# Performance work log

Hardware: AMD Instinct MI355X
Metric: run time of the kernel (lower is better)

Reference implementation:

```python
import jax, jax.numpy as jnp
import numpy as np

DIM = 256
N_EMBED = 2048
EPS_LOG = 1e-07


def setup_inputs() -> dict:
    key = jax.random.key(0)
    k_in, k_emb = jax.random.split(key)
    inp = jax.random.normal(k_in, (16, 64, 64, DIM), dtype=jnp.float32)
    # embeddings_initial_variance = 1 -> plain randn
    embed = jax.random.normal(k_emb, (DIM, N_EMBED), dtype=jnp.float32)
    return {"input": inp, "embed": embed}


def reference(input, embed):
    # Eval-mode forward of Quantize (no EMA buffer updates).
    flatten = input.reshape(-1, DIM)                      # [N, dim]
    # squared euclidean distance via expansion:
    dist = (
        jnp.sum(flatten * flatten, axis=1, keepdims=True)
        - 2.0 * (flatten @ embed)
        + jnp.sum(embed * embed, axis=0, keepdims=True)
    )
    embed_ind_flat = jnp.argmax(-dist, axis=1)            # [N] int
    embed_ind = embed_ind_flat.reshape(input.shape[:-1])  # [B,H,W]

    # gather codes: F.embedding(embed_ind, embed.T)
    quantize = jnp.take(embed.T, embed_ind, axis=0)       # [B,H,W,dim]

    # commitment loss with detached quantize
    diff = jnp.mean((jax.lax.stop_gradient(quantize) - input) ** 2)

    # straight-through estimator
    quantize_st = input + jax.lax.stop_gradient(quantize - input)

    # perplexity from average code assignment probabilities
    n = flatten.shape[0]
    counts = jnp.zeros((N_EMBED,), dtype=flatten.dtype).at[embed_ind_flat].add(1.0)
    avg_probas = counts / n
    perplexity = jnp.exp(
        -jnp.sum(avg_probas * jnp.log(jnp.clip(avg_probas, EPS_LOG, None)))
    )
    return quantize_st, diff, embed_ind, perplexity
```

## Files before the change

### kernel.cpp

```cpp
#include <hip/hip_runtime.h>
#include <cstdint>
#include <cstddef>

#define DIM    256
#define NE     2048
#define NROWS  65536

#define OFF_DIFF ((size_t)16777216)
#define OFF_IND  ((size_t)16777217)
#define OFF_PERP ((size_t)16842753)

#define WS_DIFF   0
#define WS_CNT    64
#define WS_EN     8256
#define WS_ET     16448
#define WS_BPH    2113600
#define WS_BPL    3162176
#define WS_NEED_V2 ((size_t)4210752)
#define WS_ET_NEED ((size_t)2113600)

typedef __attribute__((ext_vector_type(8))) _Float16 half8;
typedef __attribute__((ext_vector_type(4))) float    float4v;

__device__ __forceinline__ float4v mfma16(half8 a, half8 b, float4v c) {
    return __builtin_amdgcn_mfma_f32_16x16x32_f16(a, b, c, 0, 0, 0);
}

__device__ __forceinline__ void gld16(const void* g, void* l) {
    __builtin_amdgcn_global_load_lds((const __attribute__((address_space(1))) void*)g,
                                     (__attribute__((address_space(3))) void*)l,
                                     16, 0, 0);
}


__global__ __launch_bounds__(256) void k_prep(const float* __restrict__ embed,
                                              float* __restrict__ enorm) {
    int j = blockIdx.x * 256 + threadIdx.x;
    double s = 0.0;
    for (int d = 0; d < DIM; ++d) {
        float e = embed[(size_t)d * NE + j];
        s += (double)e * (double)e;
    }
    enorm[j] = (float)s;
}

__global__ __launch_bounds__(256) void k_transpose(const float* __restrict__ embed,
                                                   float* __restrict__ embedT) {
    int j0 = blockIdx.x * 8;
    for (int jj = 0; jj < 8; ++jj) {
        int j = j0 + jj;
        embedT[(size_t)j * DIM + threadIdx.x] = embed[(size_t)threadIdx.x * NE + j];
    }
}

__global__ __launch_bounds__(256) void k_pack(const float* __restrict__ embed,
                                              _Float16* __restrict__ bph,
                                              _Float16* __restrict__ bpl) {
    int t   = blockIdx.x * 256 + threadIdx.x;
    int col = t & (NE - 1);
    int kg  = t >> 11;
    half8 h, l;
#pragma unroll
    for (int j = 0; j < 8; ++j) {
        float e = embed[(size_t)(kg * 8 + j) * NE + col];
        _Float16 eh = (_Float16)e;
        h[j] = eh;
        l[j] = (_Float16)(e - (float)eh);
    }
    size_t idx = (size_t)(col >> 5) * 1024 + (size_t)kg * 32 + (size_t)(col & 31);
    *(half8*)(bph + idx * 8) = h;
    *(half8*)(bpl + idx * 8) = l;
}


__device__ __forceinline__ void stage_chunk(const char* srch, const char* srcl,
                                            char* dst, int w, int lane) {
#pragma unroll
    for (int s = 0; s < 4; ++s) {
        int seg = w * 4 + s;
        gld16(srch + seg * 1024 + lane * 16, dst + seg * 1024);
        gld16(srcl + seg * 1024 + lane * 16, dst + 16384 + seg * 1024);
    }
}

__global__ __launch_bounds__(256, 2) void k_gemm(
    const float* __restrict__ inp,
    const _Float16* __restrict__ bph,
    const _Float16* __restrict__ bpl,
    const float* __restrict__ enorm,
    const float* __restrict__ embedT,
    float* __restrict__ out,
    int* __restrict__ counts,
    double* __restrict__ diffacc)
{
    __shared__ __align__(16) char ldsB[2][32768];
    const int tid  = threadIdx.x;
    const int w    = tid >> 6;
    const int lane = tid & 63;
    const int q    = lane >> 4;
    const int nl   = lane & 15;
    const int m0   = blockIdx.x * 128;
    const int mw   = m0 + w * 32;

    half8 ah[2][8], al[2][8];
#pragma unroll
    for (int mf = 0; mf < 2; ++mf) {
        const float* xr = inp + (size_t)(mw + mf * 16 + nl) * DIM + q * 8;
#pragma unroll
        for (int c = 0; c < 8; ++c) {
            float4 f0 = *(const float4*)(xr + c * 32);
            float4 f1 = *(const float4*)(xr + c * 32 + 4);
            float fs[8] = {f0.x, f0.y, f0.z, f0.w, f1.x, f1.y, f1.z, f1.w};
            half8 hh, ll;
#pragma unroll
            for (int j = 0; j < 8; ++j) {
                _Float16 xh = (_Float16)fs[j];
                hh[j] = xh;
                ll[j] = (_Float16)(fs[j] - (float)xh);
            }
            ah[mf][c] = hh;
            al[mf][c] = ll;
        }
    }

    float sv1[2][4], sv2[2][4];
    int   si1[2][4], si2[2][4];
#pragma unroll
    for (int mf = 0; mf < 2; ++mf)
#pragma unroll
        for (int r = 0; r < 4; ++r) {
            sv1[mf][r] = -3.4e38f; sv2[mf][r] = -3.4e38f;
            si1[mf][r] = 0;        si2[mf][r] = 0;
        }

    stage_chunk((const char*)bph, (const char*)bpl, &ldsB[0][0], w, lane);
    __syncthreads();

    for (int nc = 0; nc < 64; ++nc) {
        int pn = nc & 1;
        if (nc < 63)
            stage_chunk((const char*)bph + (size_t)(nc + 1) * 16384,
                        (const char*)bpl + (size_t)(nc + 1) * 16384,
                        &ldsB[pn ^ 1][0], w, lane);

        const char* bb = &ldsB[pn][0] + q * 512 + nl * 16;
        float4v acc[2][2];
#pragma unroll
        for (int mf = 0; mf < 2; ++mf)
#pragma unroll
            for (int nf = 0; nf < 2; ++nf)
                acc[mf][nf] = (float4v){0.f, 0.f, 0.f, 0.f};

#pragma unroll
        for (int c = 0; c < 8; ++c) {
            half8 bh0 = *(const half8*)(bb + c * 2048);
            half8 bh1 = *(const half8*)(bb + c * 2048 + 256);
            half8 bl0 = *(const half8*)(bb + 16384 + c * 2048);
            half8 bl1 = *(const half8*)(bb + 16384 + c * 2048 + 256);
            acc[0][0] = mfma16(ah[0][c], bh0, acc[0][0]);
            acc[1][0] = mfma16(ah[1][c], bh0, acc[1][0]);
            acc[0][1] = mfma16(ah[0][c], bh1, acc[0][1]);
            acc[1][1] = mfma16(ah[1][c], bh1, acc[1][1]);
            acc[0][0] = mfma16(al[0][c], bh0, acc[0][0]);
            acc[1][0] = mfma16(al[1][c], bh0, acc[1][0]);
            acc[0][1] = mfma16(al[0][c], bh1, acc[0][1]);
            acc[1][1] = mfma16(al[1][c], bh1, acc[1][1]);
            acc[0][0] = mfma16(ah[0][c], bl0, acc[0][0]);
            acc[1][0] = mfma16(ah[1][c], bl0, acc[1][0]);
            acc[0][1] = mfma16(ah[0][c], bl1, acc[0][1]);
            acc[1][1] = mfma16(ah[1][c], bl1, acc[1][1]);
        }

        int colb = nc * 32;
#pragma unroll
        for (int nf = 0; nf < 2; ++nf) {
            int col = colb + nf * 16 + nl;
            float en05 = -0.5f * enorm[col];
#pragma unroll
            for (int mf = 0; mf < 2; ++mf) {
#pragma unroll
                for (int r = 0; r < 4; ++r) {
                    float s  = acc[mf][nf][r] + en05;
                    bool g1  = (s > sv1[mf][r]);
                    bool g2  = (s > sv2[mf][r]);
                    float nb2 = g1 ? sv1[mf][r] : (g2 ? s   : sv2[mf][r]);
                    int   ni2 = g1 ? si1[mf][r] : (g2 ? col : si2[mf][r]);
                    sv1[mf][r] = g1 ? s   : sv1[mf][r];
                    si1[mf][r] = g1 ? col : si1[mf][r];
                    sv2[mf][r] = nb2;
                    si2[mf][r] = ni2;
                }
            }
        }
        __syncthreads();
    }

#pragma unroll
    for (int mf = 0; mf < 2; ++mf)
#pragma unroll
        for (int r = 0; r < 4; ++r) {
            float v1 = sv1[mf][r], v2 = sv2[mf][r];
            int   i1 = si1[mf][r], i2 = si2[mf][r];
#pragma unroll
            for (int msk = 1; msk < 16; msk <<= 1) {
                float ov1 = __shfl_xor(v1, msk); int oi1 = __shfl_xor(i1, msk);
                float ov2 = __shfl_xor(v2, msk); int oi2 = __shfl_xor(i2, msk);
                bool afirst = (v1 > ov1) || (v1 == ov1 && i1 < oi1);
                float cv = afirst ? ov1 : v1;  int ci = afirst ? oi1 : i1;
                float sv = afirst ? v2  : ov2; int si = afirst ? i2  : oi2;
                v1 = afirst ? v1 : ov1;        i1 = afirst ? i1 : oi1;
                bool sfirst = (sv > cv) || (sv == cv && si < ci);
                v2 = sfirst ? sv : cv;         i2 = sfirst ? si : ci;
            }
            si1[mf][r] = i1;
            si2[mf][r] = i2;
        }

    double dsum = 0.0;
#pragma unroll
    for (int mf = 0; mf < 2; ++mf)
#pragma unroll
        for (int qq = 0; qq < 4; ++qq)
#pragma unroll
            for (int r = 0; r < 4; ++r) {
                int i1 = __shfl(si1[mf][r], qq * 16);
                int i2 = __shfl(si2[mf][r], qq * 16);
                int row = mw + mf * 16 + qq * 4 + r;
                float4 xv = *(const float4*)(inp    + (size_t)row * DIM + lane * 4);
                float4 e1 = *(const float4*)(embedT + (size_t)i1  * DIM + lane * 4);
                float4 e2 = *(const float4*)(embedT + (size_t)i2  * DIM + lane * 4);
                float d1 = xv.x * e1.x + xv.y * e1.y + xv.z * e1.z + xv.w * e1.w;
                float d2 = xv.x * e2.x + xv.y * e2.y + xv.z * e2.z + xv.w * e2.w;
#pragma unroll
                for (int msk = 1; msk < 64; msk <<= 1) {
                    d1 += __shfl_xor(d1, msk);
                    d2 += __shfl_xor(d2, msk);
                }
                float s1 = 2.f * d1 - enorm[i1];
                float s2 = 2.f * d2 - enorm[i2];
                bool take2 = (s2 > s1) || (s2 == s1 && i2 < i1);
                int win = take2 ? i2 : i1;
                float4 qv = take2 ? e2 : e1;
                *(float4*)(out + (size_t)row * DIM + lane * 4) = qv;
                float dx = qv.x - xv.x, dy = qv.y - xv.y;
                float dz = qv.z - xv.z, dw = qv.w - xv.w;
                dsum += (double)(dx * dx + dy * dy + dz * dz + dw * dw);
                if (lane == 0) {
                    out[OFF_IND + row] = (float)win;
                    atomicAdd(&counts[win], 1);
                }
            }
#pragma unroll
    for (int msk = 1; msk < 64; msk <<= 1) dsum += __shfl_xor(dsum, msk);
    if (lane == 0) atomicAdd(diffacc, dsum);
}

__global__ __launch_bounds__(256) void k_main(const float* __restrict__ inp,
                                              const float* __restrict__ embed,
                                              const float* __restrict__ enorm,
                                              const float* __restrict__ embedT,
                                              int useT,
                                              float* __restrict__ out,
                                              int* __restrict__ counts,
                                              double* __restrict__ diffacc) {
    __shared__ float XsT[DIM][64];
    const int tid = threadIdx.x;
    const int m0  = blockIdx.x * 64;
#pragma unroll
    for (int i = 0; i < 16; ++i) {
        int f = tid + 256 * i;
        int row = f >> 6, c4 = f & 63;
        float4 v = *(const float4*)&inp[(size_t)(m0 + row) * DIM + c4 * 4];
        XsT[c4 * 4 + 0][row] = v.x; XsT[c4 * 4 + 1][row] = v.y;
        XsT[c4 * 4 + 2][row] = v.z; XsT[c4 * 4 + 3][row] = v.w;
    }
    __syncthreads();
    const int tx = tid & 15, ty = tid >> 4;
    float bv[4]; int bi[4];
#pragma unroll
    for (int mi = 0; mi < 4; ++mi) { bv[mi] = -1e30f; bi[mi] = 0x7fffffff; }
    for (int n0 = 0; n0 < NE; n0 += 64) {
        float acc[4][4] = {};
        const float* bp = embed + n0 + tx * 4;
        const float* ap = &XsT[0][ty * 4];
#pragma unroll 8
        for (int k = 0; k < DIM; ++k) {
            float4 b4 = *(const float4*)(bp + (size_t)k * NE);
            float4 a4 = *(const float4*)(ap + k * 64);
            acc[0][0] = fmaf(a4.x, b4.x, acc[0][0]); acc[0][1] = fmaf(a4.x, b4.y, acc[0][1]);
            acc[0][2] = fmaf(a4.x, b4.z, acc[0][2]); acc[0][3] = fmaf(a4.x, b4.w, acc[0][3]);
            acc[1][0] = fmaf(a4.y, b4.x, acc[1][0]); acc[1][1] = fmaf(a4.y, b4.y, acc[1][1]);
            acc[1][2] = fmaf(a4.y, b4.z, acc[1][2]); acc[1][3] = fmaf(a4.y, b4.w, acc[1][3]);
            acc[2][0] = fmaf(a4.z, b4.x, acc[2][0]); acc[2][1] = fmaf(a4.z, b4.y, acc[2][1]);
            acc[2][2] = fmaf(a4.z, b4.z, acc[2][2]); acc[2][3] = fmaf(a4.z, b4.w, acc[2][3]);
            acc[3][0] = fmaf(a4.w, b4.x, acc[3][0]); acc[3][1] = fmaf(a4.w, b4.y, acc[3][1]);
            acc[3][2] = fmaf(a4.w, b4.z, acc[3][2]); acc[3][3] = fmaf(a4.w, b4.w, acc[3][3]);
        }
        float4 en4 = *(const float4*)&enorm[n0 + tx * 4];
        int c0 = n0 + tx * 4;
#pragma unroll
        for (int mi = 0; mi < 4; ++mi) {
            float s0 = 2.f * acc[mi][0] - en4.x, s1 = 2.f * acc[mi][1] - en4.y;
            float s2 = 2.f * acc[mi][2] - en4.z, s3 = 2.f * acc[mi][3] - en4.w;
            float v = s0; int idx = c0;
            if (s1 > v) { v = s1; idx = c0 + 1; }
            if (s2 > v) { v = s2; idx = c0 + 2; }
            if (s3 > v) { v = s3; idx = c0 + 3; }
#pragma unroll
            for (int o = 1; o < 16; o <<= 1) {
                float ov = __shfl_xor(v, o, 64); int oi = __shfl_xor(idx, o, 64);
                if (ov > v || (ov == v && oi < idx)) { v = ov; idx = oi; }
            }
            if (v > bv[mi] || (v == bv[mi] && idx < bi[mi])) { bv[mi] = v; bi[mi] = idx; }
        }
    }
    __syncthreads();
    int* sidx = (int*)&XsT[0][0];
    if (tx == 0) {
#pragma unroll
        for (int mi = 0; mi < 4; ++mi) {
            int rl = ty * 4 + mi; int idx = bi[mi];
            sidx[rl] = idx;
            out[OFF_IND + m0 + rl] = (float)idx;
            atomicAdd(&counts[idx], 1);
        }
    }
    __syncthreads();
    float dsum = 0.f;
    for (int rl = 0; rl < 64; ++rl) {
        int idx = sidx[rl];
        float qv = useT ? embedT[(size_t)idx * DIM + tid] : embed[(size_t)tid * NE + idx];
        float x = inp[(size_t)(m0 + rl) * DIM + tid];
        out[(size_t)(m0 + rl) * DIM + tid] = qv;
        float d = qv - x;
        dsum = fmaf(d, d, dsum);
    }
    double ds = (double)dsum;
#pragma unroll
    for (int o = 32; o > 0; o >>= 1) ds += __shfl_down(ds, o, 64);
    double* red = (double*)&XsT[4][0];
    if ((tid & 63) == 0) red[tid >> 6] = ds;
    __syncthreads();
    if (tid == 0) atomicAdd(diffacc, red[0] + red[1] + red[2] + red[3]);
}

__global__ __launch_bounds__(256) void k_fin(const int* __restrict__ counts,
                                             const double* __restrict__ diffacc,
                                             float* __restrict__ out) {
    __shared__ double red[4];
    int tid = threadIdx.x;
    double s = 0.0;
    for (int i = tid; i < NE; i += 256) {
        int c = counts[i];
        if (c > 0) {
            float p = (float)c * (1.0f / 65536.0f);
            s += (double)(p * logf(p));
        }
    }
#pragma unroll
    for (int o = 32; o > 0; o >>= 1) s += __shfl_down(s, o, 64);
    if ((tid & 63) == 0) red[tid >> 6] = s;
    __syncthreads();
    if (tid == 0) {
        double t = red[0] + red[1] + red[2] + red[3];
        out[OFF_PERP] = expf((float)(-t));
        out[OFF_DIFF] = (float)(diffacc[0] * (1.0 / 16777216.0));
    }
}

extern "C" void kernel_launch(void* const* d_in, const int* in_sizes, int n_in,
                              void* d_out, int out_size, void* d_ws, size_t ws_size,
                              hipStream_t stream) {
    (void)in_sizes; (void)n_in; (void)out_size;
    const float* inp   = (const float*)d_in[0];
    const float* embed = (const float*)d_in[1];
    float* out = (float*)d_out;
    char*  ws  = (char*)d_ws;

    double*   diffacc = (double*)(ws + WS_DIFF);
    int*      counts  = (int*)(ws + WS_CNT);
    float*    enorm   = (float*)(ws + WS_EN);
    float*    embedT  = (float*)(ws + WS_ET);
    _Float16* bph     = (_Float16*)(ws + WS_BPH);
    _Float16* bpl     = (_Float16*)(ws + WS_BPL);

    hipMemsetAsync(d_ws, 0, 8256, stream);
    k_prep<<<NE / 256, 256, 0, stream>>>(embed, enorm);

    if (ws_size >= WS_NEED_V2) {
        k_transpose<<<DIM, 256, 0, stream>>>(embed, embedT);
        k_pack<<<NE * 32 / 256, 256, 0, stream>>>(embed, bph, bpl);
        k_gemm<<<NROWS / 128, 256, 0, stream>>>(inp, bph, bpl, enorm, embedT,
                                                out, counts, diffacc);
    } else {
        int useT = (ws_size >= WS_ET_NEED) ? 1 : 0;
        if (useT) k_transpose<<<DIM, 256, 0, stream>>>(embed, embedT);
        k_main<<<NROWS / 64, 256, 0, stream>>>(inp, embed, enorm,
                                               useT ? embedT : embed, useT,
                                               out, counts, diffacc);
    }
    k_fin<<<1, 256, 0, stream>>>(counts, diffacc, out);
}
```

Measured before the change: 319.9 us.

## Switch GEMM to 32x32x16 MFMA with packed int top-2 argmax and fused pack/transpose

Replaces the 16x16x32 MFMA tiling with 32x32x16 MFMA, so each wave computes a 32x32 tile per chunk with a single accumulator. Fragments are read from a single packed hi/lo buffer. The running top-2 search now packs a quantized score and the column index into one int, which turns compare-and-select into integer max/min operations. The per-code norm offset is precomputed into LDS. The transpose kernel is merged into the pack kernel. The risks are coarse score quantization, which leans on the exact top-2 rescoring, and higher register pressure from 16-element accumulators and 32 A fragments.

```diff
diff --git a/kernel.cpp b/kernel.cpp
--- a/kernel.cpp
+++ b/kernel.cpp
@@ -13,17 +13,16 @@
 #define WS_DIFF   0
 #define WS_CNT    64
 #define WS_EN     8256
-#define WS_ET     16448
-#define WS_BPH    2113600
-#define WS_BPL    3162176
-#define WS_NEED_V2 ((size_t)4210752)
-#define WS_ET_NEED ((size_t)2113600)
-
-typedef __attribute__((ext_vector_type(8))) _Float16 half8;
-typedef __attribute__((ext_vector_type(4))) float    float4v;
-
-__device__ __forceinline__ float4v mfma16(half8 a, half8 b, float4v c) {
-    return __builtin_amdgcn_mfma_f32_16x16x32_f16(a, b, c, 0, 0, 0);
+#define WS_ENC    16448
+#define WS_ET     24640
+#define WS_BPK    2121792
+#define WS_NEED_V2 ((size_t)(2121792 + 2097152))
+
+typedef __attribute__((ext_vector_type(8)))  _Float16 half8;
+typedef __attribute__((ext_vector_type(16))) float    float16v;
+
+__device__ __forceinline__ float16v mfma32(half8 a, half8 b, float16v c) {
+    return __builtin_amdgcn_mfma_f32_32x32x16_f16(a, b, c, 0, 0, 0);
 }
 
 __device__ __forceinline__ void gld16(const void* g, void* l) {
@@ -34,82 +33,72 @@
 
 
 __global__ __launch_bounds__(256) void k_prep(const float* __restrict__ embed,
-                                              float* __restrict__ enorm) {
+                                              float* __restrict__ enorm,
+                                              float* __restrict__ enc) {
     int j = blockIdx.x * 256 + threadIdx.x;
     double s = 0.0;
     for (int d = 0; d < DIM; ++d) {
         float e = embed[(size_t)d * NE + j];
         s += (double)e * (double)e;
     }
-    enorm[j] = (float)s;
-}
-
-__global__ __launch_bounds__(256) void k_transpose(const float* __restrict__ embed,
-                                                   float* __restrict__ embedT) {
-    int j0 = blockIdx.x * 8;
-    for (int jj = 0; jj < 8; ++jj) {
-        int j = j0 + jj;
-        embedT[(size_t)j * DIM + threadIdx.x] = embed[(size_t)threadIdx.x * NE + j];
-    }
+    float en = (float)s;
+    enorm[j] = en;
+    enc[j]   = (128.0f - 0.5f * en) * 2048.0f;
 }
 
 __global__ __launch_bounds__(256) void k_pack(const float* __restrict__ embed,
-                                              _Float16* __restrict__ bph,
-                                              _Float16* __restrict__ bpl) {
-    int t   = blockIdx.x * 256 + threadIdx.x;
-    int col = t & (NE - 1);
-    int kg  = t >> 11;
+                                              _Float16* __restrict__ bpk,
+                                              float* __restrict__ embedT) {
+    int tt    = blockIdx.x * 256 + threadIdx.x;
+    int nc    = tt >> 10;
+    int tfrag = (tt >> 6) & 15;
+    int lane  = tt & 63;
+    int col   = nc * 32 + (lane & 31);
+    int k0    = tfrag * 16 + (lane >> 5) * 8;
     half8 h, l;
 #pragma unroll
     for (int j = 0; j < 8; ++j) {
-        float e = embed[(size_t)(kg * 8 + j) * NE + col];
+        float e = embed[(size_t)(k0 + j) * NE + col];
         _Float16 eh = (_Float16)e;
         h[j] = eh;
         l[j] = (_Float16)(e - (float)eh);
-    }
-    size_t idx = (size_t)(col >> 5) * 1024 + (size_t)kg * 32 + (size_t)(col & 31);
-    *(half8*)(bph + idx * 8) = h;
-    *(half8*)(bpl + idx * 8) = l;
-}
-
-
-__device__ __forceinline__ void stage_chunk(const char* srch, const char* srcl,
-                                            char* dst, int w, int lane) {
-#pragma unroll
-    for (int s = 0; s < 4; ++s) {
-        int seg = w * 4 + s;
-        gld16(srch + seg * 1024 + lane * 16, dst + seg * 1024);
-        gld16(srcl + seg * 1024 + lane * 16, dst + 16384 + seg * 1024);
-    }
-}
+        embedT[(size_t)col * DIM + k0 + j] = e;
+    }
+    char* base = (char*)bpk + (size_t)nc * 32768 + (size_t)tfrag * 1024 + (size_t)lane * 16;
+    *(half8*)(base)         = h;
+    *(half8*)(base + 16384) = l;
+}
+
 
 __global__ __launch_bounds__(256, 2) void k_gemm(
     const float* __restrict__ inp,
-    const _Float16* __restrict__ bph,
-    const _Float16* __restrict__ bpl,
+    const _Float16* __restrict__ bpk,
     const float* __restrict__ enorm,
+    const float* __restrict__ enc,
     const float* __restrict__ embedT,
     float* __restrict__ out,
     int* __restrict__ counts,
     double* __restrict__ diffacc)
 {
     __shared__ __align__(16) char ldsB[2][32768];
+    __shared__ float encs[NE];
     const int tid  = threadIdx.x;
     const int w    = tid >> 6;
     const int lane = tid & 63;
-    const int q    = lane >> 4;
-    const int nl   = lane & 15;
-    const int m0   = blockIdx.x * 128;
-    const int mw   = m0 + w * 32;
-
-    half8 ah[2][8], al[2][8];
-#pragma unroll
-    for (int mf = 0; mf < 2; ++mf) {
-        const float* xr = inp + (size_t)(mw + mf * 16 + nl) * DIM + q * 8;
-#pragma unroll
-        for (int c = 0; c < 8; ++c) {
-            float4 f0 = *(const float4*)(xr + c * 32);
-            float4 f1 = *(const float4*)(xr + c * 32 + 4);
+    const int kh   = lane >> 5;
+    const int m    = lane & 31;
+    const int mw   = blockIdx.x * 128 + w * 32;
+
+#pragma unroll
+    for (int i = 0; i < 8; ++i) encs[tid + 256 * i] = enc[tid + 256 * i];
+
+    half8 ah[16], al[16];
+    {
+        const float* xr = inp + (size_t)(mw + m) * DIM + kh * 8;
+#pragma unroll
+        for (int t = 0; t < 16; ++t) {
+            float4 f0 = *(const float4*)(xr + t * 16);
+            float4 f1 = *(const float4*)(xr + t * 16 + 4);
             float fs[8] = {f0.x, f0.y, f0.z, f0.w, f1.x, f1.y, f1.z, f1.w};
             half8 hh, ll;
 #pragma unroll
@@ -118,138 +107,111 @@
                 hh[j] = xh;
                 ll[j] = (_Float16)(fs[j] - (float)xh);
             }
-            ah[mf][c] = hh;
-            al[mf][c] = ll;
-        }
-    }
-
-    float sv1[2][4], sv2[2][4];
-    int   si1[2][4], si2[2][4];
-#pragma unroll
-    for (int mf = 0; mf < 2; ++mf)
-#pragma unroll
-        for (int r = 0; r < 4; ++r) {
-            sv1[mf][r] = -3.4e38f; sv2[mf][r] = -3.4e38f;
-            si1[mf][r] = 0;        si2[mf][r] = 0;
-        }
-
-    stage_chunk((const char*)bph, (const char*)bpl, &ldsB[0][0], w, lane);
+            ah[t] = hh;
+            al[t] = ll;
+        }
+    }
+
+    int P1[16], P2[16];
+#pragma unroll
+    for (int r = 0; r < 16; ++r) { P1[r] = (int)0x80000000; P2[r] = (int)0x80000000; }
+
+    {
+        const char* src = (const char*)bpk;
+#pragma unroll
+        for (int s = 0; s < 8; ++s) {
+            int seg = w * 8 + s;
+            gld16(src + seg * 1024 + lane * 16, &ldsB[0][0] + seg * 1024);
+        }
+    }
     __syncthreads();
 
     for (int nc = 0; nc < 64; ++nc) {
         int pn = nc & 1;
-        if (nc < 63)
-            stage_chunk((const char*)bph + (size_t)(nc + 1) * 16384,
-                        (const char*)bpl + (size_t)(nc + 1) * 16384,
-                        &ldsB[pn ^ 1][0], w, lane);
-
-        const char* bb = &ldsB[pn][0] + q * 512 + nl * 16;
-        float4v acc[2][2];
-#pragma unroll
-        for (int mf = 0; mf < 2; ++mf)
-#pragma unroll
-            for (int nf = 0; nf < 2; ++nf)
-                acc[mf][nf] = (float4v){0.f, 0.f, 0.f, 0.f};
-
-#pragma unroll
-        for (int c = 0; c < 8; ++c) {
-            half8 bh0 = *(const half8*)(bb + c * 2048);
-            half8 bh1 = *(const half8*)(bb + c * 2048 + 256);
-            half8 bl0 = *(const half8*)(bb + 16384 + c * 2048);
-            half8 bl1 = *(const half8*)(bb + 16384 + c * 2048 + 256);
-            acc[0][0] = mfma16(ah[0][c], bh0, acc[0][0]);
-            acc[1][0] = mfma16(ah[1][c], bh0, acc[1][0]);
-            acc[0][1] = mfma16(ah[0][c], bh1, acc[0][1]);
-            acc[1][1] = mfma16(ah[1][c], bh1, acc[1][1]);
-            acc[0][0] = mfma16(al[0][c], bh0, acc[0][0]);
-            acc[1][0] = mfma16(al[1][c], bh0, acc[1][0]);
-            acc[0][1] = mfma16(al[0][c], bh1, acc[0][1]);
-            acc[1][1] = mfma16(al[1][c], bh1, acc[1][1]);
-            acc[0][0] = mfma16(ah[0][c], bl0, acc[0][0]);
-            acc[1][0] = mfma16(ah[1][c], bl0, acc[1][0]);
-            acc[0][1] = mfma16(ah[0][c], bl1, acc[0][1]);
-            acc[1][1] = mfma16(ah[1][c], bl1, acc[1][1]);
-        }
-
-        int colb = nc * 32;
-#pragma unroll
-        for (int nf = 0; nf < 2; ++nf) {
-            int col = colb + nf * 16 + nl;
-            float en05 = -0.5f * enorm[col];
-#pragma unroll
-            for (int mf = 0; mf < 2; ++mf) {
-#pragma unroll
-                for (int r = 0; r < 4; ++r) {
-                    float s  = acc[mf][nf][r] + en05;
-                    bool g1  = (s > sv1[mf][r]);
-                    bool g2  = (s > sv2[mf][r]);
-                    float nb2 = g1 ? sv1[mf][r] : (g2 ? s   : sv2[mf][r]);
-                    int   ni2 = g1 ? si1[mf][r] : (g2 ? col : si2[mf][r]);
-                    sv1[mf][r] = g1 ? s   : sv1[mf][r];
-                    si1[mf][r] = g1 ? col : si1[mf][r];
-                    sv2[mf][r] = nb2;
-                    si2[mf][r] = ni2;
-                }
+        if (nc < 63) {
+            const char* src = (const char*)bpk + (size_t)(nc + 1) * 32768;
+            char* dst = &ldsB[pn ^ 1][0];
+#pragma unroll
+            for (int s = 0; s < 8; ++s) {
+                int seg = w * 8 + s;
+                gld16(src + seg * 1024 + lane * 16, dst + seg * 1024);
             }
         }
+
+        float en = encs[nc * 32 + m];
+        const char* bb = &ldsB[pn][0] + lane * 16;
+
+        float16v acc = {};
+#pragma unroll
+        for (int t = 0; t < 16; ++t) {
+            half8 bh = *(const half8*)(bb + t * 1024);
+            half8 bl = *(const half8*)(bb + 16384 + t * 1024);
+            acc = mfma32(ah[t], bh, acc);
+            acc = mfma32(al[t], bh, acc);
+            acc = mfma32(ah[t], bl, acc);
+        }
+
+        int colp = nc * 32 + m;
+#pragma unroll
+        for (int r = 0; r < 16; ++r) {
+            float sf = fmaf(acc[r], 2048.0f, en);
+            sf = __builtin_amdgcn_fmed3f(sf, -1048064.0f, 1048064.0f);
+            int si = (int)sf;
+            int p  = (int)(((unsigned)si << 11) | (unsigned)colp);
+            int mn = (P1[r] < p) ? P1[r] : p;
+            P2[r]  = (P2[r] > mn) ? P2[r] : mn;
+            P1[r]  = (P1[r] > p) ? P1[r] : p;
+        }
         __syncthreads();
     }
 
 #pragma unroll
-    for (int mf = 0; mf < 2; ++mf)
-#pragma unroll
-        for (int r = 0; r < 4; ++r) {
-            float v1 = sv1[mf][r], v2 = sv2[mf][r];
-            int   i1 = si1[mf][r], i2 = si2[mf][r];
-#pragma unroll
-            for (int msk = 1; msk < 16; msk <<= 1) {
-                float ov1 = __shfl_xor(v1, msk); int oi1 = __shfl_xor(i1, msk);
-                float ov2 = __shfl_xor(v2, msk); int oi2 = __shfl_xor(i2, msk);
-                bool afirst = (v1 > ov1) || (v1 == ov1 && i1 < oi1);
-                float cv = afirst ? ov1 : v1;  int ci = afirst ? oi1 : i1;
-                float sv = afirst ? v2  : ov2; int si = afirst ? i2  : oi2;
-                v1 = afirst ? v1 : ov1;        i1 = afirst ? i1 : oi1;
-                bool sfirst = (sv > cv) || (sv == cv && si < ci);
-                v2 = sfirst ? sv : cv;         i2 = sfirst ? si : ci;
-            }
-            si1[mf][r] = i1;
-            si2[mf][r] = i2;
-        }
+    for (int r = 0; r < 16; ++r) {
+        int p1 = P1[r], p2 = P2[r];
+#pragma unroll
+        for (int msk = 1; msk < 32; msk <<= 1) {
+            int o1 = __shfl_xor(p1, msk);
+            int o2 = __shfl_xor(p2, msk);
+            int mx2 = (p2 > o2) ? p2 : o2;
+            int mn1 = (p1 < o1) ? p1 : o1;
+            p2 = (mx2 > mn1) ? mx2 : mn1;
+            p1 = (p1 > o1) ? p1 : o1;
+        }
+        P1[r] = p1; P2[r] = p2;
+    }
 
     double dsum = 0.0;
 #pragma unroll
-    for (int mf = 0; mf < 2; ++mf)
-#pragma unroll
-        for (int qq = 0; qq < 4; ++qq)
-#pragma unroll
-            for (int r = 0; r < 4; ++r) {
-                int i1 = __shfl(si1[mf][r], qq * 16);
-                int i2 = __shfl(si2[mf][r], qq * 16);
-                int row = mw + mf * 16 + qq * 4 + r;
-                float4 xv = *(const float4*)(inp    + (size_t)row * DIM + lane * 4);
-                float4 e1 = *(const float4*)(embedT + (size_t)i1  * DIM + lane * 4);
-                float4 e2 = *(const float4*)(embedT + (size_t)i2  * DIM + lane * 4);
-                float d1 = xv.x * e1.x + xv.y * e1.y + xv.z * e1.z + xv.w * e1.w;
-                float d2 = xv.x * e2.x + xv.y * e2.y + xv.z * e2.z + xv.w * e2.w;
-#pragma unroll
-                for (int msk = 1; msk < 64; msk <<= 1) {
-                    d1 += __shfl_xor(d1, msk);
-                    d2 += __shfl_xor(d2, msk);
-                }
-                float s1 = 2.f * d1 - enorm[i1];
-                float s2 = 2.f * d2 - enorm[i2];
-                bool take2 = (s2 > s1) || (s2 == s1 && i2 < i1);
-                int win = take2 ? i2 : i1;
-                float4 qv = take2 ? e2 : e1;
-                *(float4*)(out + (size_t)row * DIM + lane * 4) = qv;
-                float dx = qv.x - xv.x, dy = qv.y - xv.y;
-                float dz = qv.z - xv.z, dw = qv.w - xv.w;
-                dsum += (double)(dx * dx + dy * dy + dz * dz + dw * dw);
-                if (lane == 0) {
-                    out[OFF_IND + row] = (float)win;
-                    atomicAdd(&counts[win], 1);
-                }
-            }
+    for (int rr = 0; rr < 32; ++rr) {
+        const int reg = (rr & 3) | (((rr >> 3) & 3) << 2);
+        const int src = ((rr >> 2) & 1) << 5;
+        int i1 = __shfl(P1[reg], src) & 2047;
+        int i2 = __shfl(P2[reg], src) & 2047;
+        int row = mw + rr;
+        float4 xv = *(const float4*)(inp    + (size_t)row * DIM + lane * 4);
+        float4 e1 = *(const float4*)(embedT + (size_t)i1  * DIM + lane * 4);
+        float4 e2 = *(const float4*)(embedT + (size_t)i2  * DIM + lane * 4);
+        float d1 = xv.x * e1.x + xv.y * e1.y + xv.z * e1.z + xv.w * e1.w;
+        float d2 = xv.x * e2.x + xv.y * e2.y + xv.z * e2.z + xv.w * e2.w;
+#pragma unroll
+        for (int msk = 1; msk < 64; msk <<= 1) {
+            d1 += __shfl_xor(d1, msk);
+            d2 += __shfl_xor(d2, msk);
+        }
+        float s1 = 2.f * d1 - enorm[i1];
+        float s2 = 2.f * d2 - enorm[i2];
+        bool take2 = (s2 > s1) || (s2 == s1 && i2 < i1);
+        int win = take2 ? i2 : i1;
+        float4 qv = take2 ? e2 : e1;
+        *(float4*)(out + (size_t)row * DIM + lane * 4) = qv;
+        float dx = qv.x - xv.x, dy = qv.y - xv.y;
+        float dz = qv.z - xv.z, dw = qv.w - xv.w;
+        dsum += (double)(dx * dx + dy * dy + dz * dz + dw * dw);
+        if (lane == 0) {
+            out[OFF_IND + row] = (float)win;
+            atomicAdd(&counts[win], 1);
+        }
+    }
 #pragma unroll
     for (int msk = 1; msk < 64; msk <<= 1) dsum += __shfl_xor(dsum, msk);
     if (lane == 0) atomicAdd(diffacc, dsum);
@@ -258,8 +220,6 @@
 __global__ __launch_bounds__(256) void k_main(const float* __restrict__ inp,
                                               const float* __restrict__ embed,
                                               const float* __restrict__ enorm,
-                                              const float* __restrict__ embedT,
-                                              int useT,
                                               float* __restrict__ out,
                                               int* __restrict__ counts,
                                               double* __restrict__ diffacc) {
@@ -329,7 +289,7 @@
     float dsum = 0.f;
     for (int rl = 0; rl < 64; ++rl) {
         int idx = sidx[rl];
-        float qv = useT ? embedT[(size_t)idx * DIM + tid] : embed[(size_t)tid * NE + idx];
+        float qv = embed[(size_t)tid * NE + idx];
         float x = inp[(size_t)(m0 + rl) * DIM + tid];
         out[(size_t)(m0 + rl) * DIM + tid] = qv;
         float d = qv - x;
@@ -380,23 +340,19 @@
     double*   diffacc = (double*)(ws + WS_DIFF);
     int*      counts  = (int*)(ws + WS_CNT);
     float*    enorm   = (float*)(ws + WS_EN);
+    float*    enc     = (float*)(ws + WS_ENC);
     float*    embedT  = (float*)(ws + WS_ET);
-    _Float16* bph     = (_Float16*)(ws + WS_BPH);
-    _Float16* bpl     = (_Float16*)(ws + WS_BPL);
+    _Float16* bpk     = (_Float16*)(ws + WS_BPK);
 
     hipMemsetAsync(d_ws, 0, 8256, stream);
-    k_prep<<<NE / 256, 256, 0, stream>>>(embed, enorm);
+    k_prep<<<NE / 256, 256, 0, stream>>>(embed, enorm, enc);
 
     if (ws_size >= WS_NEED_V2) {
-        k_transpose<<<DIM, 256, 0, stream>>>(embed, embedT);
-        k_pack<<<NE * 32 / 256, 256, 0, stream>>>(embed, bph, bpl);
-        k_gemm<<<NROWS / 128, 256, 0, stream>>>(inp, bph, bpl, enorm, embedT,
+        k_pack<<<256, 256, 0, stream>>>(embed, bpk, embedT);
+        k_gemm<<<NROWS / 128, 256, 0, stream>>>(inp, bpk, enorm, enc, embedT,
                                                 out, counts, diffacc);
     } else {
-        int useT = (ws_size >= WS_ET_NEED) ? 1 : 0;
-        if (useT) k_transpose<<<DIM, 256, 0, stream>>>(embed, embedT);
         k_main<<<NROWS / 64, 256, 0, stream>>>(inp, embed, enorm,
-                                               useT ? embedT : embed, useT,
                                                out, counts, diffacc);
     }
     k_fin<<<1, 256, 0, stream>>>(counts, diffacc, out);
```

Result: slower. 335.3 us (+4.8%).
